# Performance work log

Hardware: AMD Instinct MI355X
Metric: run time of the kernel (lower is better)

The kernel has to match this reference:

```python
import jax, jax.numpy as jnp
import numpy as np

SOFTENING = 0.01
SOFTENING_SQ = SOFTENING * SOFTENING


def setup_inputs() -> dict:
    key = jax.random.key(0)
    k1, k2 = jax.random.split(key)
    N = 8192
    positions = jax.random.normal(k1, (N, 3), dtype=jnp.float32)
    masses = jax.random.uniform(k2, (N,), dtype=jnp.float32)
    return {"positions": positions, "masses": masses}


def reference(positions, masses):
    # diff[i, j] = r_j - r_i  -> shape (N, N, 3)
    diff = positions[None, :, :] - positions[:, None, :]
    dist_sq = jnp.sum(diff * diff, axis=2) + SOFTENING_SQ        # (N, N)
    inv_dist_cubed = dist_sq ** (-1.5)                            # (N, N)
    # a_i = sum_j m_j * diff[i, j] * inv_dist_cubed[i, j]
    w = masses[None, :] * inv_dist_cubed                          # (N, N)
    accelerations = jnp.einsum('ij,ijd->id', w, diff)             # (N, 3)
    return accelerations
```

## Files before the change

### kernel.cpp

```cpp
#include <hip/hip_runtime.h>

#define NBODY 8192
#define BLOCK 256
#define SLABS 32
#define JCHUNK (NBODY / SLABS)
#define PHASE 16
#define NPHASE (JCHUNK / PHASE)
#define SOFT2 1.0e-4f

__global__ __launch_bounds__(BLOCK, 4) void nbody_kernel(
    const float* __restrict__ pos, const float* __restrict__ mass,
    float* __restrict__ out) {
  __shared__ float4 tile[JCHUNK];

  const int t = threadIdx.x;
  const int i = blockIdx.x * BLOCK + t;
  const int j = blockIdx.y * JCHUNK + t;

  tile[t] = make_float4(pos[j * 3 + 0], pos[j * 3 + 1], pos[j * 3 + 2],
                        mass[j]);

  const float xi = pos[i * 3 + 0];
  const float yi = pos[i * 3 + 1];
  const float zi = pos[i * 3 + 2];

  __syncthreads();

  float ax = 0.f, ay = 0.f, az = 0.f;

  for (int c = 0; c < NPHASE; ++c) {
    float4 jt[PHASE];
#pragma unroll
    for (int u = 0; u < PHASE; ++u) jt[u] = tile[c * PHASE + u];

#pragma unroll
    for (int u = 0; u < PHASE; ++u) {
      float dx = jt[u].x - xi;
      float dy = jt[u].y - yi;
      float dz = jt[u].z - zi;
      float r2 = fmaf(dx, dx, fmaf(dy, dy, fmaf(dz, dz, SOFT2)));
      float inv = __builtin_amdgcn_rsqf(r2);
      float w = jt[u].w * ((inv * inv) * inv);
      ax = fmaf(w, dx, ax);
      ay = fmaf(w, dy, ay);
      az = fmaf(w, dz, az);
    }
  }

  atomicAdd(&out[i * 3 + 0], ax);
  atomicAdd(&out[i * 3 + 1], ay);
  atomicAdd(&out[i * 3 + 2], az);
}

extern "C" void kernel_launch(void* const* d_in, const int* in_sizes, int n_in,
                              void* d_out, int out_size, void* d_ws,
                              size_t ws_size, hipStream_t stream) {
  const float* pos = (const float*)d_in[0];
  const float* mass = (const float*)d_in[1];
  float* out = (float*)d_out;

  hipMemsetAsync(d_out, 0, (size_t)out_size * sizeof(float), stream);

  nbody_kernel<<<dim3(NBODY / BLOCK, SLABS), BLOCK, 0, stream>>>(pos, mass,
                                                                 out);
}
```

Baseline: 78.50 us.

## Pack bodies into float4 workspace and stream j-tiles via double-buffered uniform loads

Adds a pack kernel that writes position and mass into one float4 array in the workspace. The force kernel then drops the shared-memory tile and the barrier. It reads j-bodies straight from global memory with block-uniform addresses, which the compiler may turn into scalar loads, and double-buffers them in registers with a smaller phase size. The goal is to take LDS traffic and synchronisation out of the compute-bound inner loop. The cost is an extra kernel launch, and the last prefetch reads past the end of each chunk, which for the final slab means past the end of the packed array.

```diff
diff --git a/kernel.cpp b/kernel.cpp
--- a/kernel.cpp
+++ b/kernel.cpp
@@ -4,47 +4,58 @@
 #define BLOCK 256
 #define SLABS 32
 #define JCHUNK (NBODY / SLABS)
-#define PHASE 16
+#define PHASE 8
 #define NPHASE (JCHUNK / PHASE)
+#define PWPAD (PHASE)
 #define SOFT2 1.0e-4f
 
-__global__ __launch_bounds__(BLOCK, 4) void nbody_kernel(
+__global__ __launch_bounds__(BLOCK) void pack_kernel(
     const float* __restrict__ pos, const float* __restrict__ mass,
+    float4* __restrict__ pw) {
+  const int i = blockIdx.x * BLOCK + threadIdx.x;
+  pw[i] = make_float4(pos[i * 3 + 0], pos[i * 3 + 1], pos[i * 3 + 2], mass[i]);
+}
+
+#define PAIR(o)                                        \
+  do {                                                 \
+    float dx = (o).x - xi;                             \
+    float dy = (o).y - yi;                             \
+    float dz = (o).z - zi;                             \
+    float r2 = fmaf(dx, dx, fmaf(dy, dy, fmaf(dz, dz, SOFT2))); \
+    float inv = __builtin_amdgcn_rsqf(r2);             \
+    float w = (o).w * ((inv * inv) * inv);             \
+    ax = fmaf(w, dx, ax);                              \
+    ay = fmaf(w, dy, ay);                              \
+    az = fmaf(w, dz, az);                              \
+  } while (0)
+
+__global__ __launch_bounds__(BLOCK, 4) void force_kernel(
+    const float4* __restrict__ pw, const float* __restrict__ pos,
     float* __restrict__ out) {
-  __shared__ float4 tile[JCHUNK];
-
   const int t = threadIdx.x;
   const int i = blockIdx.x * BLOCK + t;
-  const int j = blockIdx.y * JCHUNK + t;
-
-  tile[t] = make_float4(pos[j * 3 + 0], pos[j * 3 + 1], pos[j * 3 + 2],
-                        mass[j]);
+  const float4* __restrict__ pj = pw + blockIdx.y * JCHUNK;
 
   const float xi = pos[i * 3 + 0];
   const float yi = pos[i * 3 + 1];
   const float zi = pos[i * 3 + 2];
 
-  __syncthreads();
-
   float ax = 0.f, ay = 0.f, az = 0.f;
 
-  for (int c = 0; c < NPHASE; ++c) {
-    float4 jt[PHASE];
+  float4 A[PHASE], B[PHASE];
 #pragma unroll
-    for (int u = 0; u < PHASE; ++u) jt[u] = tile[c * PHASE + u];
+  for (int u = 0; u < PHASE; ++u) A[u] = pj[u];
 
+  for (int c = 0; c < NPHASE; c += 2) {
 #pragma unroll
-    for (int u = 0; u < PHASE; ++u) {
-      float dx = jt[u].x - xi;
-      float dy = jt[u].y - yi;
-      float dz = jt[u].z - zi;
-      float r2 = fmaf(dx, dx, fmaf(dy, dy, fmaf(dz, dz, SOFT2)));
-      float inv = __builtin_amdgcn_rsqf(r2);
-      float w = jt[u].w * ((inv * inv) * inv);
-      ax = fmaf(w, dx, ax);
-      ay = fmaf(w, dy, ay);
-      az = fmaf(w, dz, az);
-    }
+    for (int u = 0; u < PHASE; ++u) B[u] = pj[(c + 1) * PHASE + u];
+#pragma unroll
+    for (int u = 0; u < PHASE; ++u) PAIR(A[u]);
+#pragma unroll
+    for (int u = 0; u < PHASE; ++u)
+      A[u] = pj[(c + 2) * PHASE + u];
+#pragma unroll
+    for (int u = 0; u < PHASE; ++u) PAIR(B[u]);
   }
 
   atomicAdd(&out[i * 3 + 0], ax);
@@ -58,9 +69,10 @@
   const float* pos = (const float*)d_in[0];
   const float* mass = (const float*)d_in[1];
   float* out = (float*)d_out;
+  float4* pw = (float4*)d_ws;
 
   hipMemsetAsync(d_out, 0, (size_t)out_size * sizeof(float), stream);
 
-  nbody_kernel<<<dim3(NBODY / BLOCK, SLABS), BLOCK, 0, stream>>>(pos, mass,
-                                                                 out);
+  pack_kernel<<<NBODY / BLOCK, BLOCK, 0, stream>>>(pos, mass, pw);
+  force_kernel<<<dim3(NBODY / BLOCK, SLABS), BLOCK, 0, stream>>>(pw, pos, out);
 }
```

Result: slower. 83.14 us (+5.9%).

## Expand pairwise distance algebraically to drop per-pair subtractions

Applied to the files above, without the earlier changes.

Rewrites r2 as |ri|^2 + |rj|^2 - 2 ri·rj using precomputed -2*rj and |rj|^2+soft in shared memory. The force sum is split into sum(W*(-2rj)) plus a 2*sum(W)*ri correction applied once at the end, with masses pre-scaled by -0.5 in a separate shared array. This removes the three per-pair subtractions and saves VALU work in the inner loop. In exchange it adds an extra LDS read stream and risks cancellation error when bodies are close or far from the origin.

```diff
diff --git a/kernel.cpp b/kernel.cpp
--- a/kernel.cpp
+++ b/kernel.cpp
@@ -12,44 +12,61 @@
     const float* __restrict__ pos, const float* __restrict__ mass,
     float* __restrict__ out) {
   __shared__ float4 tile[JCHUNK];
+  __shared__ float4 mmt[JCHUNK / 4];
 
   const int t = threadIdx.x;
   const int i = blockIdx.x * BLOCK + t;
   const int j = blockIdx.y * JCHUNK + t;
 
-  tile[t] = make_float4(pos[j * 3 + 0], pos[j * 3 + 1], pos[j * 3 + 2],
-                        mass[j]);
+  {
+    const float jx = pos[j * 3 + 0];
+    const float jy = pos[j * 3 + 1];
+    const float jz = pos[j * 3 + 2];
+    tile[t] = make_float4(-2.f * jx, -2.f * jy, -2.f * jz,
+                          fmaf(jx, jx, fmaf(jy, jy, fmaf(jz, jz, SOFT2))));
+    if (t < JCHUNK / 4) {
+      const int jb = blockIdx.y * JCHUNK + 4 * t;
+      mmt[t] = make_float4(-0.5f * mass[jb + 0], -0.5f * mass[jb + 1],
+                           -0.5f * mass[jb + 2], -0.5f * mass[jb + 3]);
+    }
+  }
 
   const float xi = pos[i * 3 + 0];
   const float yi = pos[i * 3 + 1];
   const float zi = pos[i * 3 + 2];
+  const float ni = fmaf(xi, xi, fmaf(yi, yi, zi * zi));
 
   __syncthreads();
 
-  float ax = 0.f, ay = 0.f, az = 0.f;
+  float Sx = 0.f, Sy = 0.f, Sz = 0.f, sw = 0.f;
 
   for (int c = 0; c < NPHASE; ++c) {
     float4 jt[PHASE];
+    float4 mm[PHASE / 4];
 #pragma unroll
     for (int u = 0; u < PHASE; ++u) jt[u] = tile[c * PHASE + u];
+#pragma unroll
+    for (int u = 0; u < PHASE / 4; ++u) mm[u] = mmt[c * (PHASE / 4) + u];
+    const float* mmf = (const float*)mm;
 
 #pragma unroll
     for (int u = 0; u < PHASE; ++u) {
-      float dx = jt[u].x - xi;
-      float dy = jt[u].y - yi;
-      float dz = jt[u].z - zi;
-      float r2 = fmaf(dx, dx, fmaf(dy, dy, fmaf(dz, dz, SOFT2)));
+      float r2 = fmaf(jt[u].x, xi,
+                 fmaf(jt[u].y, yi,
+                 fmaf(jt[u].z, zi, fmaf(jt[u].w, 1.0f, ni))));
       float inv = __builtin_amdgcn_rsqf(r2);
-      float w = jt[u].w * ((inv * inv) * inv);
-      ax = fmaf(w, dx, ax);
-      ay = fmaf(w, dy, ay);
-      az = fmaf(w, dz, az);
+      float W = mmf[u] * ((inv * inv) * inv);
+      Sx = fmaf(W, jt[u].x, Sx);
+      Sy = fmaf(W, jt[u].y, Sy);
+      Sz = fmaf(W, jt[u].z, Sz);
+      sw = fmaf(W, 1.0f, sw);
     }
   }
 
-  atomicAdd(&out[i * 3 + 0], ax);
-  atomicAdd(&out[i * 3 + 1], ay);
-  atomicAdd(&out[i * 3 + 2], az);
+  const float s2 = sw + sw;
+  atomicAdd(&out[i * 3 + 0], fmaf(s2, xi, Sx));
+  atomicAdd(&out[i * 3 + 1], fmaf(s2, yi, Sy));
+  atomicAdd(&out[i * 3 + 2], fmaf(s2, zi, Sz));
 }
 
 extern "C" void kernel_launch(void* const* d_in, const int* in_sizes, int n_in,
```

Result: no change. 78.31 us (-0.2%).
